# Optimization experiments

Hardware: AMD Instinct MI355X
Metric: run time of the kernel (lower is better)

## Reference

```python
import jax, jax.numpy as jnp
import numpy as np

D_MODEL = 1024
NUM_HEADS = 16
HEAD_DIM = D_MODEL // NUM_HEADS
CLAMP = 1e9


def setup_inputs() -> dict:
    key = jax.random.key(0)
    ks = jax.random.split(key, 5)
    B, S = 2, 2048
    x = jax.random.normal(ks[0], (B, S, D_MODEL), dtype=jnp.float32)
    # causal mask, broadcastable over [B, H, S, S]
    mask = jnp.tril(jnp.ones((S, S), dtype=bool))
    Wqkv = jax.random.normal(ks[1], (D_MODEL, 3 * D_MODEL), dtype=jnp.float32) * (1.0 / np.sqrt(D_MODEL))
    bqkv = jax.random.normal(ks[2], (3 * D_MODEL,), dtype=jnp.float32) * 0.02
    Wo = jax.random.normal(ks[3], (D_MODEL, D_MODEL), dtype=jnp.float32) * (1.0 / np.sqrt(D_MODEL))
    bo = jax.random.normal(ks[4], (D_MODEL,), dtype=jnp.float32) * 0.02
    return {"x": x, "mask": mask, "Wqkv": Wqkv, "bqkv": bqkv, "Wo": Wo, "bo": bo}


def reference(x, mask, Wqkv, bqkv, Wo, bo):
    B, S, _ = x.shape
    qkv = x @ Wqkv + bqkv                               # [B, S, 3*d_model]
    qkv = qkv.reshape(B, S, NUM_HEADS, 3 * HEAD_DIM).transpose(0, 2, 1, 3)  # [B, H, S, 3*hd]
    q, k, v = jnp.split(qkv, 3, axis=-1)                # each [B, H, S, hd]
    scale = 1.0 / np.sqrt(HEAD_DIM)
    scores = jnp.einsum('bhqd,bhkd->bhqk', q, k) * scale  # [B, H, S, S]
    scores = jnp.where(mask, scores, -jnp.inf)
    scores = jnp.clip(scores, -CLAMP, CLAMP)
    attn = jax.nn.softmax(scores, axis=-1)
    values = jnp.einsum('bhqk,bhkd->bhqd', attn, v)     # [B, H, S, hd]
    values = values.transpose(0, 2, 1, 3).reshape(B, S, D_MODEL)
    return values @ Wo + bo
```

## Files before the change

kernel.cpp:

```cpp
#include <hip/hip_runtime.h>
#include <hip/hip_bf16.h>

#define S_LEN 2048
#define NHEAD 16
#define HDIM  64
#define DMODEL 1024

typedef unsigned short u16;
typedef __attribute__((ext_vector_type(8))) short short8;
typedef __attribute__((ext_vector_type(4))) float floatx4;
typedef __attribute__((ext_vector_type(4))) u16 u16x4;

__device__ __forceinline__ u16 f2bf(float f) {
  unsigned u = __builtin_bit_cast(unsigned, f);
  u += 0x7fffu + ((u >> 16) & 1u);
  return (u16)(u >> 16);
}
__device__ __forceinline__ float bf2f(u16 b) {
  unsigned u = ((unsigned)b) << 16;
  return __builtin_bit_cast(float, u);
}
__device__ __forceinline__ void gload_lds16(const void* g, void* l) {
  __builtin_amdgcn_global_load_lds((const __attribute__((address_space(1))) unsigned int*)g,
                                   (__attribute__((address_space(3))) unsigned int*)l,
                                   16, 0, 0);
}
__device__ __forceinline__ int swz(int b) { return b ^ (((b >> 7) & 7) << 4); }

#define MFMA16(a, b, c) __builtin_amdgcn_mfma_f32_16x16x32_bf16(a, b, c, 0, 0, 0)

__global__ __launch_bounds__(256) void k_prep(const float* __restrict__ x,
                                              const float* __restrict__ Wqkv,
                                              const float* __restrict__ Wo,
                                              u16* __restrict__ xh,
                                              u16* __restrict__ wh,
                                              u16* __restrict__ woh) {
  int bid = blockIdx.x, tid = threadIdx.x;
  if (bid < 4096) {
    int i = (bid * 256 + tid) * 4;
    float4 v = *(const float4*)(x + i);
    u16x4 hv = {f2bf(v.x), f2bf(v.y), f2bf(v.z), f2bf(v.w)};
    *(u16x4*)(xh + i) = hv;
    return;
  }
  __shared__ float t[32][33];
  const float* in; u16* oh; int C, bx, by;
  if (bid < 7168) { int b = bid - 4096; in = Wqkv; oh = wh;  C = 3072; bx = b % 96; by = b / 96; }
  else            { int b = bid - 7168; in = Wo;   oh = woh; C = 1024; bx = b & 31; by = b >> 5; }
  const int R = 1024;
  int c0 = bx * 32, r0 = by * 32;
  int tx = tid & 31, ty = tid >> 5;
#pragma unroll
  for (int rr = ty; rr < 32; rr += 8) t[rr][tx] = in[(size_t)(r0 + rr) * C + c0 + tx];
  __syncthreads();
#pragma unroll
  for (int rr = ty; rr < 32; rr += 8)
    oh[(size_t)(c0 + rr) * R + r0 + tx] = f2bf(t[tx][rr]);
}

__device__ __forceinline__ void gemm_main(const u16* __restrict__ A, const u16* __restrict__ B,
                                          int m0, int n0, floatx4 (&acc)[4][4],
                                          u16* sA, u16* sB) {
  const int tid = threadIdx.x, lane = tid & 63;
  const int wid = tid >> 6, wr = wid >> 1, wc = wid & 1;
  const int cl = lane & 15, hi = lane >> 4;
  const int rmask = ((cl >> 1) & 7) << 4;
  const int aoff = (wr * 4096 + cl * 64 + hi * 16) ^ rmask;
  const int boff = (wc * 4096 + cl * 64 + hi * 16) ^ rmask;
#pragma unroll
  for (int i = 0; i < 4; ++i)
#pragma unroll
    for (int j = 0; j < 4; ++j) acc[i][j] = (floatx4){0.f, 0.f, 0.f, 0.f};

  auto stage = [&](int buf, int kt) {
    int k0 = kt * 32;
#pragma unroll
    for (int it = 0; it < 2; ++it) {
      int p = (it * 256 + tid) * 16;
      int q = swz(p);
      int row = q >> 6, colb = q & 63;
      int base = buf * 8192 + (it * 256 + (tid & ~63)) * 16;
      gload_lds16((const char*)A + (size_t)(m0 + row) * 2048 + k0 * 2 + colb, (char*)sA + base);
      gload_lds16((const char*)B + (size_t)(n0 + row) * 2048 + k0 * 2 + colb, (char*)sB + base);
    }
  };
  stage(0, 0);
  __syncthreads();
  for (int kt = 0; kt < 32; ++kt) {
    int cur = kt & 1;
    if (kt + 1 < 32) stage(cur ^ 1, kt + 1);
    short8 a[4], b[4];
#pragma unroll
    for (int i = 0; i < 4; ++i) {
      a[i] = *(const short8*)((const char*)sA + cur * 8192 + aoff + i * 1024);
      b[i] = *(const short8*)((const char*)sB + cur * 8192 + boff + i * 1024);
    }
    __builtin_amdgcn_s_setprio(1);
#pragma unroll
    for (int i = 0; i < 4; ++i)
#pragma unroll
      for (int j = 0; j < 4; ++j)
        acc[i][j] = MFMA16(a[i], b[j], acc[i][j]);
    __builtin_amdgcn_s_setprio(0);
    __syncthreads();
  }
}

__device__ __forceinline__ void gemm_main_n64(const u16* __restrict__ A, const u16* __restrict__ B,
                                              int m0, int n0, floatx4 (&acc)[4][2]) {
  __shared__ __align__(16) u16 sA[2][128 * 32];
  __shared__ __align__(16) u16 sB[2][64 * 32];
  const int tid = threadIdx.x, lane = tid & 63;
  const int wid = tid >> 6, wr = wid >> 1, wc = wid & 1;
  const int cl = lane & 15, hi = lane >> 4;
  const int rmask = ((cl >> 1) & 7) << 4;
  const int aoff = (wr * 4096 + cl * 64 + hi * 16) ^ rmask;
  const int boff = (wc * 2048 + cl * 64 + hi * 16) ^ rmask;
#pragma unroll
  for (int i = 0; i < 4; ++i)
#pragma unroll
    for (int j = 0; j < 2; ++j) acc[i][j] = (floatx4){0.f, 0.f, 0.f, 0.f};

  auto stage = [&](int buf, int kt) {
    int k0 = kt * 32;
#pragma unroll
    for (int it = 0; it < 2; ++it) {
      int p = (it * 256 + tid) * 16;
      int q = swz(p);
      int row = q >> 6, colb = q & 63;
      int base = (it * 256 + (tid & ~63)) * 16;
      gload_lds16((const char*)A + (size_t)(m0 + row) * 2048 + k0 * 2 + colb, (char*)sA[buf] + base);
    }
    {
      int p = tid * 16;
      int q = swz(p);
      int row = q >> 6, colb = q & 63;
      int base = (tid & ~63) * 16;
      gload_lds16((const char*)B + (size_t)(n0 + row) * 2048 + k0 * 2 + colb, (char*)sB[buf] + base);
    }
  };
  stage(0, 0);
  __syncthreads();
  for (int kt = 0; kt < 32; ++kt) {
    int cur = kt & 1;
    if (kt + 1 < 32) stage(cur ^ 1, kt + 1);
    short8 a[4], b[2];
#pragma unroll
    for (int i = 0; i < 4; ++i)
      a[i] = *(const short8*)((const char*)sA[cur] + aoff + i * 1024);
#pragma unroll
    for (int j = 0; j < 2; ++j)
      b[j] = *(const short8*)((const char*)sB[cur] + boff + j * 1024);
    __builtin_amdgcn_s_setprio(1);
#pragma unroll
    for (int i = 0; i < 4; ++i)
#pragma unroll
      for (int j = 0; j < 2; ++j)
        acc[i][j] = MFMA16(a[i], b[j], acc[i][j]);
    __builtin_amdgcn_s_setprio(0);
    __syncthreads();
  }
}

__global__ __launch_bounds__(256) void k_qkv_gemm(const u16* __restrict__ xh,
                                                  const u16* __restrict__ wh,
                                                  const float* __restrict__ bqkv,
                                                  u16* __restrict__ Qb, u16* __restrict__ Kb,
                                                  u16* __restrict__ Vt) {
  int bid = blockIdx.y * 24 + blockIdx.x;
  int sid = (bid & 7) * 96 + (bid >> 3);
  int m0 = (sid / 24) * 128, n0 = (sid % 24) * 128;
  __shared__ __align__(16) u16 pool[18432];
  floatx4 acc[4][4];
  gemm_main(xh, wh, m0, n0, acc, pool, pool + 8192);
  const int tid = threadIdx.x, lane = tid & 63, wid = tid >> 6;
  const int wr = wid >> 1, wc = wid & 1;
  const int cl = lane & 15, hi = lane >> 4;
  const int nbase = n0 + wc * 64;
  const int h = nbase / 192;
  const int rr0 = nbase - h * 192;
  const int mb = m0 + wr * 64;
  const int b = mb >> 11, s0 = mb & 2047;
  const int bh = b * 16 + h;
  u16* buf = pool + wid * 4608;
  float bias[4];
#pragma unroll
  for (int j = 0; j < 4; ++j) bias[j] = bqkv[nbase + j * 16 + cl];
  if (rr0 < 128) {
#pragma unroll
    for (int j = 0; j < 4; ++j)
#pragma unroll
      for (int i = 0; i < 4; ++i)
#pragma unroll
        for (int r = 0; r < 4; ++r)
          buf[(i * 16 + hi * 4 + r) * 72 + j * 16 + cl] = f2bf(acc[i][j][r] + bias[j]);
    asm volatile("s_waitcnt lgkmcnt(0)" ::: "memory");
    u16* dst0 = (rr0 ? Kb : Qb) + ((size_t)bh * 2048 + s0) * 64;
#pragma unroll
    for (int k = 0; k < 8; ++k) {
      int m_l = k * 8 + (lane >> 3);
      short8 v = *(const short8*)&buf[m_l * 72 + (lane & 7) * 8];
      *(short8*)(dst0 + (size_t)m_l * 64 + (lane & 7) * 8) = v;
    }
  } else {
#pragma unroll
    for (int j = 0; j < 4; ++j)
#pragma unroll
      for (int i = 0; i < 4; ++i)
#pragma unroll
        for (int r = 0; r < 4; ++r)
          buf[(j * 16 + cl) * 72 + i * 16 + hi * 4 + r] = f2bf(acc[i][j][r] + bias[j]);
    asm volatile("s_waitcnt lgkmcnt(0)" ::: "memory");
    u16* dst0 = Vt + (size_t)bh * 64 * 2048 + s0;
#pragma unroll
    for (int k = 0; k < 8; ++k) {
      int nl = k * 8 + (lane >> 3);
      short8 v = *(const short8*)&buf[nl * 72 + (lane & 7) * 8];
      *(short8*)(dst0 + (size_t)nl * 2048 + (lane & 7) * 8) = v;
    }
  }
}

__global__ __launch_bounds__(512, 4) void k_attn(const u16* __restrict__ Qb,
                                                 const u16* __restrict__ Kb,
                                                 const u16* __restrict__ Vt,
                                                 u16* __restrict__ ao,
                                                 u16* __restrict__ pO,
                                                 float* __restrict__ pL) {
  const int bid = blockIdx.x;
  const int bh = (bid & 7) + 8 * ((bid >> 3) / 40);
  const int idx = 39 - ((bid >> 3) % 40);
  int qt, c;
  if (idx < 4)        { qt = idx;                   c = 0; }
  else if (idx < 12)  { qt = 4 + ((idx - 4) >> 1);  c = (idx - 4) & 1; }
  else if (idx < 24)  { qt = 8 + (idx - 12) / 3;    c = (idx - 12) % 3; }
  else                { qt = 12 + ((idx - 24) >> 2); c = (idx - 24) & 3; }
  const int q0 = qt * 128;
  const int tid = threadIdx.x, lane = tid & 63, wid = tid >> 6;
  const int cl = lane & 15, hi = lane >> 4;
  const int wq0 = q0 + wid * 16;
  const int myq = wq0 + cl;
  const u16* Qp = Qb + (size_t)bh * (S_LEN * HDIM);
  const u16* Kp = Kb + (size_t)bh * (S_LEN * HDIM);
  const u16* Vp = Vt + (size_t)bh * (HDIM * S_LEN);

  __shared__ __align__(16) u16 Kl[2][64 * 64];
  __shared__ __align__(16) u16 Vl[64 * 64];
  __shared__ __align__(16) u16 Pl[8][16 * 64];

  const int kvo0 = (cl * 128 + hi * 16) ^ ((cl & 7) << 4);
  const int kvo1 = kvo0 ^ 64;
  const int pmask = (cl & 7) << 4;
  const int pbw = wid * 2048 + cl * 128 + hi * 8;
  const int pbr = wid * 2048 + cl * 128 + hi * 16;

  short8 qf[2];
#pragma unroll
  for (int kf = 0; kf < 2; ++kf)
    qf[kf] = *(const short8*)&Qp[(size_t)myq * 64 + kf * 32 + hi * 8];

  floatx4 o[4];
#pragma unroll
  for (int fc = 0; fc < 4; ++fc) o[fc] = (floatx4){0.f, 0.f, 0.f, 0.f};
  float lrun = 0.f;

  const int t0 = c * 8;
  const int NTb = min(t0 + 8, 2 * qt + 2);
  const int NTw = 2 * qt + 1 + (wid >> 2);
  const float C1 = 0.125f * 1.44269504f;
  const float C2 = 16.0f * 1.44269504f;

  auto stageK = [&](int buf, int kv0) {
    int p = tid * 16;
    int q = swz(p);
    int row = q >> 7, colb = q & 127;
    int base = (tid & ~63) * 16;
    gload_lds16((const char*)Kp + (size_t)(kv0 + row) * 128 + colb, (char*)Kl[buf] + base);
  };
  auto stageV = [&](int kv0) {
    int p = tid * 16;
    int q = swz(p);
    int row = q >> 7, colb = q & 127;
    int base = (tid & ~63) * 16;
    gload_lds16((const char*)Vp + (size_t)row * 4096 + (size_t)kv0 * 2 + colb, (char*)Vl + base);
  };
  stageK(0, t0 * 64);
  stageV(t0 * 64);
  if (t0 + 1 < NTb) stageK(1, (t0 + 1) * 64);

  for (int t = t0; t < NTb; ++t) {
    int cur = (t - t0) & 1;
    if (t + 1 < NTb) asm volatile("s_waitcnt vmcnt(1)" ::: "memory");
    else             asm volatile("s_waitcnt vmcnt(0)" ::: "memory");
    __builtin_amdgcn_s_barrier();
    if (t < NTw) {
      int kv0 = t * 64;
      floatx4 sc[4];
#pragma unroll
      for (int fc = 0; fc < 4; ++fc) sc[fc] = (floatx4){0.f, 0.f, 0.f, 0.f};
      __builtin_amdgcn_s_setprio(1);
#pragma unroll
      for (int kf = 0; kf < 2; ++kf) {
        const char* kb = (const char*)Kl[cur] + (kf ? kvo1 : kvo0);
        short8 kfv[4];
#pragma unroll
        for (int fc = 0; fc < 4; ++fc)
          kfv[fc] = *(const short8*)(kb + fc * 2048);
#pragma unroll
        for (int fc = 0; fc < 4; ++fc)
          sc[fc] = MFMA16(kfv[fc], qf[kf], sc[fc]);
      }
      __builtin_amdgcn_s_setprio(0);
      auto smax = [&](bool masked) {
        float ls = 0.f;
#pragma unroll
        for (int fc = 0; fc < 4; ++fc) {
          float p0 = exp2f(sc[fc][0] * C1 - C2);
          float p1 = exp2f(sc[fc][1] * C1 - C2);
          float p2 = exp2f(sc[fc][2] * C1 - C2);
          float p3 = exp2f(sc[fc][3] * C1 - C2);
          if (masked) {
            int key = kv0 + fc * 16 + hi * 4;
            p0 = (key + 0 <= myq) ? p0 : 0.f;
            p1 = (key + 1 <= myq) ? p1 : 0.f;
            p2 = (key + 2 <= myq) ? p2 : 0.f;
            p3 = (key + 3 <= myq) ? p3 : 0.f;
          }
          unsigned r0, r1;
          asm("v_cvt_pk_bf16_f32 %0, %1, %2" : "=v"(r0) : "v"(p0), "v"(p1));
          asm("v_cvt_pk_bf16_f32 %0, %1, %2" : "=v"(r1) : "v"(p2), "v"(p3));
          uint2 rr; rr.x = r0; rr.y = r1;
          *(uint2*)((char*)Pl + ((pbw + fc * 32) ^ pmask)) = rr;
          ls += (p0 + p1) + (p2 + p3);
        }
        lrun += ls;
      };
      if (t == NTw - 1) smax(true); else smax(false);
      __builtin_amdgcn_s_setprio(1);
#pragma unroll
      for (int kf = 0; kf < 2; ++kf) {
        short8 pa = *(const short8*)((const char*)Pl + ((pbr + kf * 64) ^ pmask));
        const char* vbp = (const char*)Vl + (kf ? kvo1 : kvo0);
        short8 vb[4];
#pragma unroll
        for (int fc = 0; fc < 4; ++fc)
          vb[fc] = *(const short8*)(vbp + fc * 2048);
#pragma unroll
        for (int fc = 0; fc < 4; ++fc)
          o[fc] = MFMA16(pa, vb[fc], o[fc]);
      }
      __builtin_amdgcn_s_setprio(0);
    }
    __builtin_amdgcn_s_barrier();
    if (t + 1 < NTb) stageV((t + 1) * 64);
    if (t + 2 < NTb) stageK(cur, (t + 2) * 64);
  }
  float l = lrun;
  l += __shfl_xor(l, 16);
  l += __shfl_xor(l, 32);
  if (qt < 4) {
    const int b = bh >> 4, h = bh & 15;
#pragma unroll
    for (int j = 0; j < 4; ++j) {
      float inv = 1.f / __shfl(l, hi * 4 + j);
      int q = wq0 + hi * 4 + j;
#pragma unroll
      for (int fc = 0; fc < 4; ++fc) {
        size_t idx2 = ((size_t)b * 2048 + q) * 1024 + h * 64 + fc * 16 + cl;
        ao[idx2] = f2bf(o[fc][j] * inv);
      }
    }
  } else {
    const int slot = (bh * 12 + (qt - 4)) * 4 + c;
    u16* po = pO + (size_t)slot * 8192 + (size_t)wid * 16 * 64;
    if (hi == 0) pL[slot * 128 + wid * 16 + cl] = l;
#pragma unroll
    for (int j = 0; j < 4; ++j) {
      int row = hi * 4 + j;
#pragma unroll
      for (int fc = 0; fc < 4; ++fc)
        po[row * 64 + fc * 16 + cl] = f2bf(o[fc][j]);
    }
  }
}

__global__ __launch_bounds__(256) void k_attn_reduce(const u16* __restrict__ pO,
                                                     const float* __restrict__ pL,
                                                     u16* __restrict__ ao) {
  int e = blockIdx.x * 256 + threadIdx.x;
  int d0 = (e & 15) * 4;
  int row = (e >> 4) & 127;
  int t = e >> 11;
  int qt = 4 + t % 12;
  int bh = t / 12;
  int nch = (2 * qt + 9) >> 3;
  int slot = t * 4;
  size_t obase = (size_t)slot * 8192 + row * 64 + d0;
  float O0 = 0.f, O1 = 0.f, O2 = 0.f, O3 = 0.f, l = 0.f;
  for (int c = 0; c < nch; ++c) {
    u16x4 v = *(const u16x4*)(pO + obase + (size_t)c * 8192);
    O0 += bf2f(v.x); O1 += bf2f(v.y); O2 += bf2f(v.z); O3 += bf2f(v.w);
    l += pL[(slot + c) * 128 + row];
  }
  float inv = 1.f / l;
  u16x4 r = {f2bf(O0 * inv), f2bf(O1 * inv), f2bf(O2 * inv), f2bf(O3 * inv)};
  int b = bh >> 4, h = bh & 15;
  int q = qt * 128 + row;
  *(u16x4*)(ao + ((size_t)b * 2048 + q) * 1024 + h * 64 + d0) = r;
}

__global__ __launch_bounds__(256) void k_out_gemm(const u16* __restrict__ ao,
                                                  const u16* __restrict__ woh,
                                                  const float* __restrict__ bo, float* __restrict__ out) {
  int bid = blockIdx.x;
  int sid = (bid & 7) * 64 + (bid >> 3);
  int m0 = (sid >> 4) * 128, n0 = (sid & 15) * 64;
  floatx4 acc[4][2];
  gemm_main_n64(ao, woh, m0, n0, acc);
  const int lane = threadIdx.x & 63, wid = threadIdx.x >> 6;
  const int wr = wid >> 1, wc = wid & 1;
#pragma unroll
  for (int j = 0; j < 2; ++j) {
    int n = n0 + wc * 32 + j * 16 + (lane & 15);
    float bias = bo[n];
#pragma unroll
    for (int i = 0; i < 4; ++i) {
#pragma unroll
      for (int r = 0; r < 4; ++r) {
        int m = m0 + wr * 64 + i * 16 + (lane >> 4) * 4 + r;
        out[(size_t)m * 1024 + n] = acc[i][j][r] + bias;
      }
    }
  }
}

extern "C" void kernel_launch(void* const* d_in, const int* in_sizes, int n_in,
                              void* d_out, int out_size, void* d_ws, size_t ws_size,
                              hipStream_t stream) {
  (void)in_sizes; (void)n_in; (void)out_size; (void)ws_size;
  const float* x    = (const float*)d_in[0];
  const float* Wqkv = (const float*)d_in[2];
  const float* bqkv = (const float*)d_in[3];
  const float* Wo   = (const float*)d_in[4];
  const float* bo   = (const float*)d_in[5];
  float* out = (float*)d_out;

  u16* p = (u16*)d_ws;
  u16* xh  = p; p += 4194304;
  u16* wh  = p; p += 3145728;
  u16* woh = p; p += 1048576;
  u16* Qb  = p; p += 4194304;
  u16* Kb  = p; p += 4194304;
  u16* Vt  = p; p += 4194304;
  u16* pO  = p; p += 12582912;
  float* pL = (float*)p; p += 393216;
  u16* ao  = xh;

  k_prep<<<8192, 256, 0, stream>>>(x, Wqkv, Wo, xh, wh, woh);
  k_qkv_gemm<<<dim3(24, 32), 256, 0, stream>>>(xh, wh, bqkv, Qb, Kb, Vt);
  k_attn<<<1280, 512, 0, stream>>>(Qb, Kb, Vt, ao, pO, pL);
  k_attn_reduce<<<3072, 256, 0, stream>>>(pO, pL, ao);
  k_out_gemm<<<512, 256, 0, stream>>>(ao, woh, bo, out);
}
```

Measured before the change: 117.5 us.

## Give each attention wave two 16-row query groups and halve block threads

The attention kernel now runs 4 waves of 256 threads instead of 8 waves, and each wave handles 32 query rows as two 16-row groups. Every K and V fragment read from LDS is reused across both groups, which halves LDS reads per MFMA and doubles the MFMA work between barriers. K/V staging issues two async loads per thread and the vmcnt wait is adjusted to match. This costs more accumulator registers per wave and fewer waves per block, so latency hiding may drop, and the causal-boundary masking now applies at 32-row granularity per wave.

```diff
diff --git a/kernel.cpp b/kernel.cpp
--- a/kernel.cpp
+++ b/kernel.cpp
@@ -221,7 +221,7 @@
   }
 }
 
-__global__ __launch_bounds__(512, 4) void k_attn(const u16* __restrict__ Qb,
+__global__ __launch_bounds__(256, 4) void k_attn(const u16* __restrict__ Qb,
                                                  const u16* __restrict__ Kb,
                                                  const u16* __restrict__ Vt,
                                                  u16* __restrict__ ao,
@@ -238,51 +238,60 @@
   const int q0 = qt * 128;
   const int tid = threadIdx.x, lane = tid & 63, wid = tid >> 6;
   const int cl = lane & 15, hi = lane >> 4;
-  const int wq0 = q0 + wid * 16;
-  const int myq = wq0 + cl;
+  const int wq0 = q0 + wid * 32;
   const u16* Qp = Qb + (size_t)bh * (S_LEN * HDIM);
   const u16* Kp = Kb + (size_t)bh * (S_LEN * HDIM);
   const u16* Vp = Vt + (size_t)bh * (HDIM * S_LEN);
 
   __shared__ __align__(16) u16 Kl[2][64 * 64];
   __shared__ __align__(16) u16 Vl[64 * 64];
-  __shared__ __align__(16) u16 Pl[8][16 * 64];
+  __shared__ __align__(16) u16 Pl[4][32 * 64];
 
   const int kvo0 = (cl * 128 + hi * 16) ^ ((cl & 7) << 4);
   const int kvo1 = kvo0 ^ 64;
   const int pmask = (cl & 7) << 4;
-  const int pbw = wid * 2048 + cl * 128 + hi * 8;
-  const int pbr = wid * 2048 + cl * 128 + hi * 16;
-
-  short8 qf[2];
-#pragma unroll
-  for (int kf = 0; kf < 2; ++kf)
-    qf[kf] = *(const short8*)&Qp[(size_t)myq * 64 + kf * 32 + hi * 8];
-
-  floatx4 o[4];
-#pragma unroll
-  for (int fc = 0; fc < 4; ++fc) o[fc] = (floatx4){0.f, 0.f, 0.f, 0.f};
-  float lrun = 0.f;
+  const int pbw = wid * 4096 + cl * 128 + hi * 8;
+  const int pbr = wid * 4096 + cl * 128 + hi * 16;
+
+  short8 qf[2][2];
+#pragma unroll
+  for (int g = 0; g < 2; ++g)
+#pragma unroll
+    for (int kf = 0; kf < 2; ++kf)
+      qf[g][kf] = *(const short8*)&Qp[(size_t)(wq0 + g * 16 + cl) * 64 + kf * 32 + hi * 8];
+
+  floatx4 o[2][4];
+#pragma unroll
+  for (int g = 0; g < 2; ++g)
+#pragma unroll
+    for (int fc = 0; fc < 4; ++fc) o[g][fc] = (floatx4){0.f, 0.f, 0.f, 0.f};
+  float lrun[2] = {0.f, 0.f};
 
   const int t0 = c * 8;
   const int NTb = min(t0 + 8, 2 * qt + 2);
-  const int NTw = 2 * qt + 1 + (wid >> 2);
+  const int NTw = 2 * qt + 1 + (wid >> 1);
   const float C1 = 0.125f * 1.44269504f;
   const float C2 = 16.0f * 1.44269504f;
 
   auto stageK = [&](int buf, int kv0) {
-    int p = tid * 16;
-    int q = swz(p);
-    int row = q >> 7, colb = q & 127;
-    int base = (tid & ~63) * 16;
-    gload_lds16((const char*)Kp + (size_t)(kv0 + row) * 128 + colb, (char*)Kl[buf] + base);
+#pragma unroll
+    for (int it = 0; it < 2; ++it) {
+      int p = (it * 256 + tid) * 16;
+      int q = swz(p);
+      int row = q >> 7, colb = q & 127;
+      int base = (it * 256 + (tid & ~63)) * 16;
+      gload_lds16((const char*)Kp + (size_t)(kv0 + row) * 128 + colb, (char*)Kl[buf] + base);
+    }
   };
   auto stageV = [&](int kv0) {
-    int p = tid * 16;
-    int q = swz(p);
-    int row = q >> 7, colb = q & 127;
-    int base = (tid & ~63) * 16;
-    gload_lds16((const char*)Vp + (size_t)row * 4096 + (size_t)kv0 * 2 + colb, (char*)Vl + base);
+#pragma unroll
+    for (int it = 0; it < 2; ++it) {
+      int p = (it * 256 + tid) * 16;
+      int q = swz(p);
+      int row = q >> 7, colb = q & 127;
+      int base = (it * 256 + (tid & ~63)) * 16;
+      gload_lds16((const char*)Vp + (size_t)row * 4096 + (size_t)kv0 * 2 + colb, (char*)Vl + base);
+    }
   };
   stageK(0, t0 * 64);
   stageV(t0 * 64);
@@ -290,14 +299,16 @@
 
   for (int t = t0; t < NTb; ++t) {
     int cur = (t - t0) & 1;
-    if (t + 1 < NTb) asm volatile("s_waitcnt vmcnt(1)" ::: "memory");
+    if (t + 1 < NTb) asm volatile("s_waitcnt vmcnt(2)" ::: "memory");
     else             asm volatile("s_waitcnt vmcnt(0)" ::: "memory");
     __builtin_amdgcn_s_barrier();
     if (t < NTw) {
       int kv0 = t * 64;
-      floatx4 sc[4];
-#pragma unroll
-      for (int fc = 0; fc < 4; ++fc) sc[fc] = (floatx4){0.f, 0.f, 0.f, 0.f};
+      floatx4 sc[2][4];
+#pragma unroll
+      for (int g = 0; g < 2; ++g)
+#pragma unroll
+        for (int fc = 0; fc < 4; ++fc) sc[g][fc] = (floatx4){0.f, 0.f, 0.f, 0.f};
       __builtin_amdgcn_s_setprio(1);
 #pragma unroll
       for (int kf = 0; kf < 2; ++kf) {
@@ -307,47 +318,57 @@
         for (int fc = 0; fc < 4; ++fc)
           kfv[fc] = *(const short8*)(kb + fc * 2048);
 #pragma unroll
-        for (int fc = 0; fc < 4; ++fc)
-          sc[fc] = MFMA16(kfv[fc], qf[kf], sc[fc]);
+        for (int g = 0; g < 2; ++g)
+#pragma unroll
+          for (int fc = 0; fc < 4; ++fc)
+            sc[g][fc] = MFMA16(kfv[fc], qf[g][kf], sc[g][fc]);
       }
       __builtin_amdgcn_s_setprio(0);
       auto smax = [&](bool masked) {
-        float ls = 0.f;
-#pragma unroll
-        for (int fc = 0; fc < 4; ++fc) {
-          float p0 = exp2f(sc[fc][0] * C1 - C2);
-          float p1 = exp2f(sc[fc][1] * C1 - C2);
-          float p2 = exp2f(sc[fc][2] * C1 - C2);
-          float p3 = exp2f(sc[fc][3] * C1 - C2);
-          if (masked) {
-            int key = kv0 + fc * 16 + hi * 4;
-            p0 = (key + 0 <= myq) ? p0 : 0.f;
-            p1 = (key + 1 <= myq) ? p1 : 0.f;
-            p2 = (key + 2 <= myq) ? p2 : 0.f;
-            p3 = (key + 3 <= myq) ? p3 : 0.f;
+#pragma unroll
+        for (int g = 0; g < 2; ++g) {
+          int myq = wq0 + g * 16 + cl;
+          float ls = 0.f;
+#pragma unroll
+          for (int fc = 0; fc < 4; ++fc) {
+            float p0 = exp2f(sc[g][fc][0] * C1 - C2);
+            float p1 = exp2f(sc[g][fc][1] * C1 - C2);
+            float p2 = exp2f(sc[g][fc][2] * C1 - C2);
+            float p3 = exp2f(sc[g][fc][3] * C1 - C2);
+            if (masked) {
+              int key = kv0 + fc * 16 + hi * 4;
+              p0 = (key + 0 <= myq) ? p0 : 0.f;
+              p1 = (key + 1 <= myq) ? p1 : 0.f;
+              p2 = (key + 2 <= myq) ? p2 : 0.f;
+              p3 = (key + 3 <= myq) ? p3 : 0.f;
+            }
+            unsigned r0, r1;
+            asm("v_cvt_pk_bf16_f32 %0, %1, %2" : "=v"(r0) : "v"(p0), "v"(p1));
+            asm("v_cvt_pk_bf16_f32 %0, %1, %2" : "=v"(r1) : "v"(p2), "v"(p3));
+            uint2 rr; rr.x = r0; rr.y = r1;
+            *(uint2*)((char*)Pl + ((pbw + g * 2048 + fc * 32) ^ pmask)) = rr;
+            ls += (p0 + p1) + (p2 + p3);
           }
-          unsigned r0, r1;
-          asm("v_cvt_pk_bf16_f32 %0, %1, %2" : "=v"(r0) : "v"(p0), "v"(p1));
-          asm("v_cvt_pk_bf16_f32 %0, %1, %2" : "=v"(r1) : "v"(p2), "v"(p3));
-          uint2 rr; rr.x = r0; rr.y = r1;
-          *(uint2*)((char*)Pl + ((pbw + fc * 32) ^ pmask)) = rr;
-          ls += (p0 + p1) + (p2 + p3);
+          lrun[g] += ls;
         }
-        lrun += ls;
       };
       if (t == NTw - 1) smax(true); else smax(false);
       __builtin_amdgcn_s_setprio(1);
 #pragma unroll
       for (int kf = 0; kf < 2; ++kf) {
-        short8 pa = *(const short8*)((const char*)Pl + ((pbr + kf * 64) ^ pmask));
         const char* vbp = (const char*)Vl + (kf ? kvo1 : kvo0);
-        short8 vb[4];
+        short8 pa[2], vb[4];
+#pragma unroll
+        for (int g = 0; g < 2; ++g)
+          pa[g] = *(const short8*)((const char*)Pl + ((pbr + g * 2048 + kf * 64) ^ pmask));
 #pragma unroll
         for (int fc = 0; fc < 4; ++fc)
           vb[fc] = *(const short8*)(vbp + fc * 2048);
 #pragma unroll
-        for (int fc = 0; fc < 4; ++fc)
-          o[fc] = MFMA16(pa, vb[fc], o[fc]);
+        for (int g = 0; g < 2; ++g)
+#pragma unroll
+          for (int fc = 0; fc < 4; ++fc)
+            o[g][fc] = MFMA16(pa[g], vb[fc], o[g][fc]);
       }
       __builtin_amdgcn_s_setprio(0);
     }
@@ -355,31 +376,34 @@
     if (t + 1 < NTb) stageV((t + 1) * 64);
     if (t + 2 < NTb) stageK(cur, (t + 2) * 64);
   }
-  float l = lrun;
-  l += __shfl_xor(l, 16);
-  l += __shfl_xor(l, 32);
-  if (qt < 4) {
-    const int b = bh >> 4, h = bh & 15;
-#pragma unroll
-    for (int j = 0; j < 4; ++j) {
-      float inv = 1.f / __shfl(l, hi * 4 + j);
-      int q = wq0 + hi * 4 + j;
-#pragma unroll
-      for (int fc = 0; fc < 4; ++fc) {
-        size_t idx2 = ((size_t)b * 2048 + q) * 1024 + h * 64 + fc * 16 + cl;
-        ao[idx2] = f2bf(o[fc][j] * inv);
+#pragma unroll
+  for (int g = 0; g < 2; ++g) {
+    float l = lrun[g];
+    l += __shfl_xor(l, 16);
+    l += __shfl_xor(l, 32);
+    if (qt < 4) {
+      const int b = bh >> 4, h = bh & 15;
+#pragma unroll
+      for (int j = 0; j < 4; ++j) {
+        float inv = 1.f / __shfl(l, hi * 4 + j);
+        int q = wq0 + g * 16 + hi * 4 + j;
+#pragma unroll
+        for (int fc = 0; fc < 4; ++fc) {
+          size_t idx2 = ((size_t)b * 2048 + q) * 1024 + h * 64 + fc * 16 + cl;
+          ao[idx2] = f2bf(o[g][fc][j] * inv);
+        }
       }
-    }
-  } else {
-    const int slot = (bh * 12 + (qt - 4)) * 4 + c;
-    u16* po = pO + (size_t)slot * 8192 + (size_t)wid * 16 * 64;
-    if (hi == 0) pL[slot * 128 + wid * 16 + cl] = l;
-#pragma unroll
-    for (int j = 0; j < 4; ++j) {
-      int row = hi * 4 + j;
-#pragma unroll
-      for (int fc = 0; fc < 4; ++fc)
-        po[row * 64 + fc * 16 + cl] = f2bf(o[fc][j]);
+    } else {
+      const int slot = (bh * 12 + (qt - 4)) * 4 + c;
+      u16* po = pO + (size_t)slot * 8192 + (size_t)(wid * 32 + g * 16) * 64;
+      if (hi == 0) pL[slot * 128 + wid * 32 + g * 16 + cl] = l;
+#pragma unroll
+      for (int j = 0; j < 4; ++j) {
+        int row = hi * 4 + j;
+#pragma unroll
+        for (int fc = 0; fc < 4; ++fc)
+          po[row * 64 + fc * 16 + cl] = f2bf(o[g][fc][j]);
+      }
     }
   }
 }
@@ -458,7 +482,7 @@
 
   k_prep<<<8192, 256, 0, stream>>>(x, Wqkv, Wo, xh, wh, woh);
   k_qkv_gemm<<<dim3(24, 32), 256, 0, stream>>>(xh, wh, bqkv, Qb, Kb, Vt);
-  k_attn<<<1280, 512, 0, stream>>>(Qb, Kb, Vt, ao, pO, pL);
+  k_attn<<<1280, 256, 0, stream>>>(Qb, Kb, Vt, ao, pO, pL);
   k_attn_reduce<<<3072, 256, 0, stream>>>(pO, pL, ao);
   k_out_gemm<<<512, 256, 0, stream>>>(ao, woh, bo, out);
 }
```

New measurement: 118.0 us. No clear change (+0.4%).

## Triple-buffer K, double-buffer V, and pass P via bpermute instead of LDS

Applied to the files above, without the earlier changes.

K gets three LDS buffers and V gets two, so the next tiles are prefetched right after the top-of-loop barrier and the second barrier per iteration is removed. The P tile no longer goes through an LDS write/read round trip. It is redistributed into MFMA A-operand layout with ds_bpermute cross-lane shuffles. This trades LDS traffic and one barrier for extra bpermute instructions and more LDS for K and V buffers, which may affect occupancy.

```diff
diff --git a/kernel.cpp b/kernel.cpp
--- a/kernel.cpp
+++ b/kernel.cpp
@@ -244,15 +244,14 @@
   const u16* Kp = Kb + (size_t)bh * (S_LEN * HDIM);
   const u16* Vp = Vt + (size_t)bh * (HDIM * S_LEN);
 
-  __shared__ __align__(16) u16 Kl[2][64 * 64];
-  __shared__ __align__(16) u16 Vl[64 * 64];
-  __shared__ __align__(16) u16 Pl[8][16 * 64];
+  __shared__ __align__(16) u16 Kl[3][64 * 64];
+  __shared__ __align__(16) u16 Vl[2][64 * 64];
 
   const int kvo0 = (cl * 128 + hi * 16) ^ ((cl & 7) << 4);
   const int kvo1 = kvo0 ^ 64;
-  const int pmask = (cl & 7) << 4;
-  const int pbw = wid * 2048 + cl * 128 + hi * 8;
-  const int pbr = wid * 2048 + cl * 128 + hi * 16;
+  const int addr_a = 4 * (cl + 16 * ((2 * hi) & 3));
+  const int addr_b = 4 * (cl + 16 * ((2 * hi + 1) & 3));
+  const bool hilo = hi < 2;
 
   short8 qf[2];
 #pragma unroll
@@ -277,22 +276,23 @@
     int base = (tid & ~63) * 16;
     gload_lds16((const char*)Kp + (size_t)(kv0 + row) * 128 + colb, (char*)Kl[buf] + base);
   };
-  auto stageV = [&](int kv0) {
+  auto stageV = [&](int buf, int kv0) {
     int p = tid * 16;
     int q = swz(p);
     int row = q >> 7, colb = q & 127;
     int base = (tid & ~63) * 16;
-    gload_lds16((const char*)Vp + (size_t)row * 4096 + (size_t)kv0 * 2 + colb, (char*)Vl + base);
+    gload_lds16((const char*)Vp + (size_t)row * 4096 + (size_t)kv0 * 2 + colb, (char*)Vl[buf] + base);
   };
-  stageK(0, t0 * 64);
-  stageV(t0 * 64);
-  if (t0 + 1 < NTb) stageK(1, (t0 + 1) * 64);
+  stageK(t0 % 3, t0 * 64);
+  stageV(t0 & 1, t0 * 64);
+  if (t0 + 1 < NTb) stageK((t0 + 1) % 3, (t0 + 1) * 64);
 
   for (int t = t0; t < NTb; ++t) {
-    int cur = (t - t0) & 1;
     if (t + 1 < NTb) asm volatile("s_waitcnt vmcnt(1)" ::: "memory");
     else             asm volatile("s_waitcnt vmcnt(0)" ::: "memory");
     __builtin_amdgcn_s_barrier();
+    if (t + 1 < NTb) stageV((t + 1) & 1, (t + 1) * 64);
+    if (t + 2 < NTb) stageK((t + 2) % 3, (t + 2) * 64);
     if (t < NTw) {
       int kv0 = t * 64;
       floatx4 sc[4];
@@ -301,7 +301,7 @@
       __builtin_amdgcn_s_setprio(1);
 #pragma unroll
       for (int kf = 0; kf < 2; ++kf) {
-        const char* kb = (const char*)Kl[cur] + (kf ? kvo1 : kvo0);
+        const char* kb = (const char*)Kl[t % 3] + (kf ? kvo1 : kvo0);
         short8 kfv[4];
 #pragma unroll
         for (int fc = 0; fc < 4; ++fc)
@@ -311,6 +311,7 @@
           sc[fc] = MFMA16(kfv[fc], qf[kf], sc[fc]);
       }
       __builtin_amdgcn_s_setprio(0);
+      unsigned w8[4][2];
       auto smax = [&](bool masked) {
         float ls = 0.f;
 #pragma unroll
@@ -329,8 +330,8 @@
           unsigned r0, r1;
           asm("v_cvt_pk_bf16_f32 %0, %1, %2" : "=v"(r0) : "v"(p0), "v"(p1));
           asm("v_cvt_pk_bf16_f32 %0, %1, %2" : "=v"(r1) : "v"(p2), "v"(p3));
-          uint2 rr; rr.x = r0; rr.y = r1;
-          *(uint2*)((char*)Pl + ((pbw + fc * 32) ^ pmask)) = rr;
+          w8[fc][0] = r0;
+          w8[fc][1] = r1;
           ls += (p0 + p1) + (p2 + p3);
         }
         lrun += ls;
@@ -339,8 +340,17 @@
       __builtin_amdgcn_s_setprio(1);
 #pragma unroll
       for (int kf = 0; kf < 2; ++kf) {
-        short8 pa = *(const short8*)((const char*)Pl + ((pbr + kf * 64) ^ pmask));
-        const char* vbp = (const char*)Vl + (kf ? kvo1 : kvo0);
+        unsigned pw[4];
+#pragma unroll
+        for (int t4 = 0; t4 < 4; ++t4) {
+          int addr = (t4 < 2) ? addr_a : addr_b;
+          unsigned lo = (unsigned)__builtin_amdgcn_ds_bpermute(addr, (int)w8[2 * kf][t4 & 1]);
+          unsigned h2 = (unsigned)__builtin_amdgcn_ds_bpermute(addr, (int)w8[2 * kf + 1][t4 & 1]);
+          pw[t4] = hilo ? lo : h2;
+        }
+        uint4 pv_ = {pw[0], pw[1], pw[2], pw[3]};
+        short8 pa = __builtin_bit_cast(short8, pv_);
+        const char* vbp = (const char*)Vl[t & 1] + (kf ? kvo1 : kvo0);
         short8 vb[4];
 #pragma unroll
         for (int fc = 0; fc < 4; ++fc)
@@ -351,9 +361,6 @@
       }
       __builtin_amdgcn_s_setprio(0);
     }
-    __builtin_amdgcn_s_barrier();
-    if (t + 1 < NTb) stageV((t + 1) * 64);
-    if (t + 2 < NTb) stageK(cur, (t + 2) * 64);
   }
   float l = lrun;
   l += __shfl_xor(l, 16);
```

Measured after the change: 124.1 us. +5.6%, slower.

## Enlarge QKV GEMM tiles to 256x256 with 512 threads and K-step 64

Applied to the files above, without the earlier changes.

Rewrites the QKV projection GEMM so each block computes a 256x256 output tile with 8 waves, 8x4 MFMA fragments per wave, and a K-step of 64 held in 128KB of double-buffered LDS. A wider swizzle suits the 128-byte rows, and the barrier is placed after a vmcnt wait. The goal is more operand reuse per LDS load and fewer barriers per unit of MFMA work. The cost is a grid of only 192 blocks, fewer than the CU count, plus heavy register and LDS use that limits occupancy to one block per CU.

```diff
diff --git a/kernel.cpp b/kernel.cpp
--- a/kernel.cpp
+++ b/kernel.cpp
@@ -26,6 +26,7 @@
                                    16, 0, 0);
 }
 __device__ __forceinline__ int swz(int b) { return b ^ (((b >> 7) & 7) << 4); }
+__device__ __forceinline__ int swz64(int b) { return b ^ (((b >> 7) & 7) << 4); }
 
 #define MFMA16(a, b, c) __builtin_amdgcn_mfma_f32_16x16x32_bf16(a, b, c, 0, 0, 0)
 
@@ -58,51 +59,125 @@
     oh[(size_t)(c0 + rr) * R + r0 + tx] = f2bf(t[tx][rr]);
 }
 
-__device__ __forceinline__ void gemm_main(const u16* __restrict__ A, const u16* __restrict__ B,
-                                          int m0, int n0, floatx4 (&acc)[4][4],
-                                          u16* sA, u16* sB) {
-  const int tid = threadIdx.x, lane = tid & 63;
-  const int wid = tid >> 6, wr = wid >> 1, wc = wid & 1;
+__global__ __launch_bounds__(512, 2) void k_qkv_gemm(const u16* __restrict__ xh,
+                                                     const u16* __restrict__ wh,
+                                                     const float* __restrict__ bqkv,
+                                                     u16* __restrict__ Qb, u16* __restrict__ Kb,
+                                                     u16* __restrict__ Vt) {
+  int bid = blockIdx.x;
+  int sid = (bid & 7) * 24 + (bid >> 3);
+  int m0 = (sid / 12) * 256, n0 = (sid % 12) * 256;
+  const int tid = threadIdx.x, lane = tid & 63, wid = tid >> 6;
   const int cl = lane & 15, hi = lane >> 4;
-  const int rmask = ((cl >> 1) & 7) << 4;
-  const int aoff = (wr * 4096 + cl * 64 + hi * 16) ^ rmask;
-  const int boff = (wc * 4096 + cl * 64 + hi * 16) ^ rmask;
-#pragma unroll
-  for (int i = 0; i < 4; ++i)
-#pragma unroll
-    for (int j = 0; j < 4; ++j) acc[i][j] = (floatx4){0.f, 0.f, 0.f, 0.f};
-
-  auto stage = [&](int buf, int kt) {
-    int k0 = kt * 32;
-#pragma unroll
-    for (int it = 0; it < 2; ++it) {
-      int p = (it * 256 + tid) * 16;
-      int q = swz(p);
-      int row = q >> 6, colb = q & 63;
-      int base = buf * 8192 + (it * 256 + (tid & ~63)) * 16;
-      gload_lds16((const char*)A + (size_t)(m0 + row) * 2048 + k0 * 2 + colb, (char*)sA + base);
-      gload_lds16((const char*)B + (size_t)(n0 + row) * 2048 + k0 * 2 + colb, (char*)sB + base);
+  const int wr = wid >> 2, wcn = wid & 3;
+
+  __shared__ __align__(16) u16 pool[65536];
+
+  auto stageKt = [&](int kt) {
+    int s = kt & 1;
+#pragma unroll
+    for (int h = 0; h < 2; ++h) {
+#pragma unroll
+      for (int it = 0; it < 2; ++it) {
+        int p = (it * 512 + tid) * 16;
+        int q = swz(p);
+        int row = q >> 7, colb = q & 127;
+        int base = (it * 512 + (tid & ~63)) * 16;
+        gload_lds16((const char*)xh + (size_t)(m0 + h * 128 + row) * 2048 + kt * 128 + colb,
+                    (char*)pool + s * 32768 + h * 16384 + base);
+        gload_lds16((const char*)wh + (size_t)(n0 + h * 128 + row) * 2048 + kt * 128 + colb,
+                    (char*)pool + 65536 + s * 32768 + h * 16384 + base);
+      }
     }
   };
-  stage(0, 0);
+
+  const int mask = (cl & 7) << 4;
+  const int aoff = (cl * 128 + hi * 16) ^ mask;
+  const int boff = (wcn & 1) * 8192 + ((cl * 128 + hi * 16) ^ mask);
+  const char* Abase = (const char*)pool + wr * 16384;
+  const char* Bbase = (const char*)pool + 65536 + (wcn >> 1) * 16384;
+
+  floatx4 acc[8][4];
+#pragma unroll
+  for (int f = 0; f < 8; ++f)
+#pragma unroll
+    for (int j = 0; j < 4; ++j) acc[f][j] = (floatx4){0.f, 0.f, 0.f, 0.f};
+
+  stageKt(0);
+  for (int kt = 0; kt < 16; ++kt) {
+    int s = kt & 1;
+    asm volatile("s_waitcnt vmcnt(0)" ::: "memory");
+    __builtin_amdgcn_s_barrier();
+    if (kt + 1 < 16) stageKt(kt + 1);
+    const char* Ab = Abase + s * 32768;
+    const char* Bb = Bbase + s * 32768;
+    short8 bfr[4][2];
+#pragma unroll
+    for (int j = 0; j < 4; ++j) {
+      bfr[j][0] = *(const short8*)(Bb + boff + j * 2048);
+      bfr[j][1] = *(const short8*)(Bb + (boff ^ 64) + j * 2048);
+    }
+    __builtin_amdgcn_s_setprio(1);
+#pragma unroll
+    for (int f = 0; f < 8; ++f) {
+      short8 a0 = *(const short8*)(Ab + aoff + f * 2048);
+      short8 a1 = *(const short8*)(Ab + (aoff ^ 64) + f * 2048);
+#pragma unroll
+      for (int j = 0; j < 4; ++j) acc[f][j] = MFMA16(a0, bfr[j][0], acc[f][j]);
+#pragma unroll
+      for (int j = 0; j < 4; ++j) acc[f][j] = MFMA16(a1, bfr[j][1], acc[f][j]);
+    }
+    __builtin_amdgcn_s_setprio(0);
+  }
   __syncthreads();
-  for (int kt = 0; kt < 32; ++kt) {
-    int cur = kt & 1;
-    if (kt + 1 < 32) stage(cur ^ 1, kt + 1);
-    short8 a[4], b[4];
-#pragma unroll
-    for (int i = 0; i < 4; ++i) {
-      a[i] = *(const short8*)((const char*)sA + cur * 8192 + aoff + i * 1024);
-      b[i] = *(const short8*)((const char*)sB + cur * 8192 + boff + i * 1024);
-    }
-    __builtin_amdgcn_s_setprio(1);
-#pragma unroll
-    for (int i = 0; i < 4; ++i)
-#pragma unroll
-      for (int j = 0; j < 4; ++j)
-        acc[i][j] = MFMA16(a[i], b[j], acc[i][j]);
-    __builtin_amdgcn_s_setprio(0);
-    __syncthreads();
+
+  const int nbase = n0 + wcn * 64;
+  const int h = nbase / 192;
+  const int rr0 = nbase - h * 192;
+  float bias[4];
+#pragma unroll
+  for (int j = 0; j < 4; ++j) bias[j] = bqkv[nbase + j * 16 + cl];
+  u16* buf = (u16*)((char*)pool + wid * 9216);
+#pragma unroll
+  for (int c2 = 0; c2 < 2; ++c2) {
+    const int mb = m0 + wr * 128 + c2 * 64;
+    const int b = mb >> 11, s0 = mb & 2047;
+    const int bh = b * 16 + h;
+    if (rr0 < 128) {
+#pragma unroll
+      for (int fl = 0; fl < 4; ++fl)
+#pragma unroll
+        for (int j = 0; j < 4; ++j)
+#pragma unroll
+          for (int r = 0; r < 4; ++r)
+            buf[(fl * 16 + hi * 4 + r) * 72 + j * 16 + cl] =
+                f2bf(acc[c2 * 4 + fl][j][r] + bias[j]);
+      asm volatile("s_waitcnt lgkmcnt(0)" ::: "memory");
+      u16* dst0 = (rr0 ? Kb : Qb) + ((size_t)bh * 2048 + s0) * 64;
+#pragma unroll
+      for (int k = 0; k < 8; ++k) {
+        int m_l = k * 8 + (lane >> 3);
+        short8 v = *(const short8*)&buf[m_l * 72 + (lane & 7) * 8];
+        *(short8*)(dst0 + (size_t)m_l * 64 + (lane & 7) * 8) = v;
+      }
+    } else {
+#pragma unroll
+      for (int fl = 0; fl < 4; ++fl)
+#pragma unroll
+        for (int j = 0; j < 4; ++j)
+#pragma unroll
+          for (int r = 0; r < 4; ++r)
+            buf[(j * 16 + cl) * 72 + fl * 16 + hi * 4 + r] =
+                f2bf(acc[c2 * 4 + fl][j][r] + bias[j]);
+      asm volatile("s_waitcnt lgkmcnt(0)" ::: "memory");
+      u16* dst0 = Vt + (size_t)bh * 64 * 2048 + s0;
+#pragma unroll
+      for (int k = 0; k < 8; ++k) {
+        int nl = k * 8 + (lane >> 3);
+        short8 v = *(const short8*)&buf[nl * 72 + (lane & 7) * 8];
+        *(short8*)(dst0 + (size_t)nl * 2048 + (lane & 7) * 8) = v;
+      }
+    }
   }
 }
 
@@ -126,14 +201,14 @@
 #pragma unroll
     for (int it = 0; it < 2; ++it) {
       int p = (it * 256 + tid) * 16;
-      int q = swz(p);
+      int q = swz64(p);
       int row = q >> 6, colb = q & 63;
       int base = (it * 256 + (tid & ~63)) * 16;
       gload_lds16((const char*)A + (size_t)(m0 + row) * 2048 + k0 * 2 + colb, (char*)sA[buf] + base);
     }
     {
       int p = tid * 16;
-      int q = swz(p);
+      int q = swz64(p);
       int row = q >> 6, colb = q & 63;
       int base = (tid & ~63) * 16;
       gload_lds16((const char*)B + (size_t)(n0 + row) * 2048 + k0 * 2 + colb, (char*)sB[buf] + base);
@@ -159,65 +234,6 @@
         acc[i][j] = MFMA16(a[i], b[j], acc[i][j]);
     __builtin_amdgcn_s_setprio(0);
     __syncthreads();
-  }
-}
-
-__global__ __launch_bounds__(256) void k_qkv_gemm(const u16* __restrict__ xh,
-                                                  const u16* __restrict__ wh,
-                                                  const float* __restrict__ bqkv,
-                                                  u16* __restrict__ Qb, u16* __restrict__ Kb,
-                                                  u16* __restrict__ Vt) {
-  int bid = blockIdx.y * 24 + blockIdx.x;
-  int sid = (bid & 7) * 96 + (bid >> 3);
-  int m0 = (sid / 24) * 128, n0 = (sid % 24) * 128;
-  __shared__ __align__(16) u16 pool[18432];
-  floatx4 acc[4][4];
-  gemm_main(xh, wh, m0, n0, acc, pool, pool + 8192);
-  const int tid = threadIdx.x, lane = tid & 63, wid = tid >> 6;
-  const int wr = wid >> 1, wc = wid & 1;
-  const int cl = lane & 15, hi = lane >> 4;
-  const int nbase = n0 + wc * 64;
-  const int h = nbase / 192;
-  const int rr0 = nbase - h * 192;
-  const int mb = m0 + wr * 64;
-  const int b = mb >> 11, s0 = mb & 2047;
-  const int bh = b * 16 + h;
-  u16* buf = pool + wid * 4608;
-  float bias[4];
-#pragma unroll
-  for (int j = 0; j < 4; ++j) bias[j] = bqkv[nbase + j * 16 + cl];
-  if (rr0 < 128) {
-#pragma unroll
-    for (int j = 0; j < 4; ++j)
-#pragma unroll
-      for (int i = 0; i < 4; ++i)
-#pragma unroll
-        for (int r = 0; r < 4; ++r)
-          buf[(i * 16 + hi * 4 + r) * 72 + j * 16 + cl] = f2bf(acc[i][j][r] + bias[j]);
-    asm volatile("s_waitcnt lgkmcnt(0)" ::: "memory");
-    u16* dst0 = (rr0 ? Kb : Qb) + ((size_t)bh * 2048 + s0) * 64;
-#pragma unroll
-    for (int k = 0; k < 8; ++k) {
-      int m_l = k * 8 + (lane >> 3);
-      short8 v = *(const short8*)&buf[m_l * 72 + (lane & 7) * 8];
-      *(short8*)(dst0 + (size_t)m_l * 64 + (lane & 7) * 8) = v;
-    }
-  } else {
-#pragma unroll
-    for (int j = 0; j < 4; ++j)
-#pragma unroll
-      for (int i = 0; i < 4; ++i)
-#pragma unroll
-        for (int r = 0; r < 4; ++r)
-          buf[(j * 16 + cl) * 72 + i * 16 + hi * 4 + r] = f2bf(acc[i][j][r] + bias[j]);
-    asm volatile("s_waitcnt lgkmcnt(0)" ::: "memory");
-    u16* dst0 = Vt + (size_t)bh * 64 * 2048 + s0;
-#pragma unroll
-    for (int k = 0; k < 8; ++k) {
-      int nl = k * 8 + (lane >> 3);
-      short8 v = *(const short8*)&buf[nl * 72 + (lane & 7) * 8];
-      *(short8*)(dst0 + (size_t)nl * 2048 + (lane & 7) * 8) = v;
-    }
   }
 }
 
@@ -457,7 +473,7 @@
   u16* ao  = xh;
 
   k_prep<<<8192, 256, 0, stream>>>(x, Wqkv, Wo, xh, wh, woh);
-  k_qkv_gemm<<<dim3(24, 32), 256, 0, stream>>>(xh, wh, bqkv, Qb, Kb, Vt);
+  k_qkv_gemm<<<192, 512, 0, stream>>>(xh, wh, bqkv, Qb, Kb, Vt);
   k_attn<<<1280, 512, 0, stream>>>(Qb, Kb, Vt, ao, pO, pL);
   k_attn_reduce<<<3072, 256, 0, stream>>>(pO, pL, ao);
   k_out_gemm<<<512, 256, 0, stream>>>(ao, woh, bo, out);
```

New measurement: 111.1 us. 1.06x faster.
